# Kernel tuning notes

Hardware: AMD Instinct MI355X
Metric: run time of the kernel (lower is better)

The kernel has to match this reference:

```python
import jax, jax.numpy as jnp
import numpy as np
import math

B, S, D = 2, 8192, 1024
NW, SHIFT = 16, 256          # num_windows, shift_window
NH, DH = 16, 64              # heads = D // dim_head
DFF = 4 * D
EPS = 1e-6


def setup_inputs() -> dict:
    key = jax.random.key(0)
    ks = jax.random.split(key, 12)
    s = 1.0 / math.sqrt(D)
    return {
        "x": jax.random.normal(ks[0], (B, S, D), jnp.float32),
        "wq": jax.random.normal(ks[1], (D, NH * DH), jnp.float32) * s,
        "wk": jax.random.normal(ks[2], (D, NH * DH), jnp.float32) * s,
        "wv": jax.random.normal(ks[3], (D, NH * DH), jnp.float32) * s,
        "wo": jax.random.normal(ks[4], (NH * DH, D), jnp.float32) * s,
        "g_attn": jnp.ones((D,), jnp.float32),
        "g_ff": jnp.ones((D,), jnp.float32),
        "w1": jax.random.normal(ks[5], (D, DFF), jnp.float32) * s,
        "b1": jnp.zeros((DFF,), jnp.float32),
        "w2": jax.random.normal(ks[6], (DFF, D), jnp.float32) * (1.0 / math.sqrt(DFF)),
        "b2": jnp.zeros((D,), jnp.float32),
    }


def _rmsnorm(x, g):
    return x * g * jax.lax.rsqrt(jnp.mean(x * x, axis=-1, keepdims=True) + EPS)


def reference(x, wq, wk, wv, wo, g_attn, g_ff, w1, b1, w2, b2):
    skip = x
    h = _rmsnorm(x, g_attn)
    # shift (note: source rolls by -shift both before AND after attention)
    h = jnp.roll(h, -SHIFT, axis=1)
    # window partition: [B, NW, n, D]
    n = S // NW
    h = h.reshape(B, NW, n, D)
    q = (h @ wq).reshape(B, NW, n, NH, DH)
    k = (h @ wk).reshape(B, NW, n, NH, DH)
    v = (h @ wv).reshape(B, NW, n, NH, DH)
    scores = jnp.einsum('bwqhd,bwkhd->bwhqk', q, k) * (1.0 / math.sqrt(DH))
    a = jax.nn.softmax(scores, axis=-1)
    o = jnp.einsum('bwhqk,bwkhd->bwqhd', a, v).reshape(B, NW, n, NH * DH)
    o = (o @ wo).reshape(B, S, D)
    o = jnp.roll(o, -SHIFT, axis=1)  # faithful to source (rolls -shift again)
    x = o + skip
    skip = x
    h = _rmsnorm(x, g_ff)
    h = jax.nn.gelu(h @ w1 + b1) @ w2 + b2
    return h + skip
```

## Files before the change

### kernel.cpp

```cpp
#include <hip/hip_runtime.h>
#include <stdint.h>

#define S_LEN 8192
#define D_DIM 1024
#define SHIFT_W 256
#define NROWS 16384

typedef __bf16 bf16;
typedef __bf16 bf16x8 __attribute__((ext_vector_type(8)));
typedef __bf16 bf16x4 __attribute__((ext_vector_type(4)));
typedef float f32x4 __attribute__((ext_vector_type(4)));

typedef __attribute__((address_space(1))) const void gas_t;
typedef __attribute__((address_space(3))) void las_t;

__device__ __forceinline__ void load_lds16(const void* g, void* l) {
  __builtin_amdgcn_global_load_lds((gas_t*)g, (las_t*)l, 16, 0, 0);
}

__device__ __forceinline__ int xcd_swizzle(int orig, int nwg) {
  return (orig & 7) * (nwg >> 3) + (orig >> 3);
}

__global__ __launch_bounds__(256) void k_transpose_cvt(const float* __restrict__ in,
                                                       bf16* __restrict__ out,
                                                       int R, int C) {
  __shared__ float tile[32][33];
  int lx = threadIdx.x & 31, ly = threadIdx.x >> 5;
  int tc = blockIdx.x * 32, tr = blockIdx.y * 32;
#pragma unroll
  for (int i = 0; i < 4; i++)
    tile[ly + i * 8][lx] = in[(size_t)(tr + ly + i * 8) * C + tc + lx];
  __syncthreads();
#pragma unroll
  for (int i = 0; i < 4; i++)
    out[(size_t)(tc + ly + i * 8) * R + tr + lx] = (bf16)tile[lx][ly + i * 8];
}

__global__ __launch_bounds__(256) void k_rmsnorm(const float* __restrict__ x,
                                                 const float* __restrict__ g,
                                                 bf16* __restrict__ out, int shift) {
  int row = blockIdx.x;
  int b = row >> 13, r = row & (S_LEN - 1);
  int src = (b << 13) | ((r + shift) & (S_LEN - 1));
  int t = threadIdx.x;
  float4 v = *(const float4*)(x + (size_t)src * D_DIM + t * 4);
  float ss = v.x * v.x + v.y * v.y + v.z * v.z + v.w * v.w;
#pragma unroll
  for (int off = 32; off; off >>= 1) ss += __shfl_xor(ss, off);
  __shared__ float red[4];
  if ((t & 63) == 0) red[t >> 6] = ss;
  __syncthreads();
  ss = red[0] + red[1] + red[2] + red[3];
  float sc = rsqrtf(ss * (1.0f / D_DIM) + 1e-6f);
  float4 gv = *(const float4*)(g + t * 4);
  bf16x4 o;
  o[0] = (bf16)(v.x * gv.x * sc);
  o[1] = (bf16)(v.y * gv.y * sc);
  o[2] = (bf16)(v.z * gv.z * sc);
  o[3] = (bf16)(v.w * gv.w * sc);
  *(bf16x4*)(out + (size_t)row * D_DIM + t * 4) = o;
}

#define VM8 asm volatile("s_waitcnt vmcnt(8)" ::: "memory")
#define VM4 asm volatile("s_waitcnt vmcnt(4)" ::: "memory")
#define VM0 asm volatile("s_waitcnt vmcnt(0)" ::: "memory")
#define BAR __builtin_amdgcn_s_barrier()

#define STAGE(kbase, kk, dbuf)                                        \
  {                                                                   \
    const bf16* _ga = gAs + (kbase) + (kk) * 32;                      \
    const bf16* _gb = gBs + (kbase) + (kk) * 32;                      \
    char* _lb = smem + (dbuf) * 65536 + (kk) * 16384 + wv * 1024;     \
    load_lds16(_ga, _lb);                                             \
    load_lds16(_ga + 128 * (size_t)K, _lb + 8192);                    \
    load_lds16(_gb, _lb + 32768);                                     \
    load_lds16(_gb + 128 * (size_t)K, _lb + 40960);                   \
  }

#define DS_A(mh, kkof)                                                \
  {                                                                   \
    _Pragma("unroll") for (int mf = 0; mf < 4; mf++)                  \
        a[mf] = *(const bf16x8*)(Ac + (kkof) + aBase + (mh) * 4096 + mf * 1024); \
  }
#define DS_B(kkof)                                                    \
  {                                                                   \
    _Pragma("unroll") for (int nf = 0; nf < 4; nf++)                  \
        bfr[nf] = *(const bf16x8*)(Ac + (kkof) + bBase + nf * 1024);  \
  }
#define MFMA16(mh)                                                    \
  {                                                                   \
    __builtin_amdgcn_s_setprio(1);                                    \
    _Pragma("unroll") for (int mf = 0; mf < 4; mf++)                  \
        _Pragma("unroll") for (int nf = 0; nf < 4; nf++)              \
            acc[(mh) * 4 + mf][nf] = __builtin_amdgcn_mfma_f32_16x16x32_bf16( \
                a[mf], bfr[nf], acc[(mh) * 4 + mf][nf], 0, 0, 0);     \
    __builtin_amdgcn_s_setprio(0);                                    \
  }

template <int EPI>
__global__ __launch_bounds__(512, 2) void k_gemm(const bf16* __restrict__ A,
                                                 const bf16* __restrict__ BT,
                                                 bf16* __restrict__ obf,
                                                 float* __restrict__ of32,
                                                 const float* __restrict__ bias,
                                                 const float* __restrict__ skip,
                                                 int K, int ldc) {
  extern __shared__ char smem[];
  const int tid = threadIdx.x;
  const int wv = tid >> 6, lane = tid & 63;
  const int lr = lane & 15, lg = lane >> 4;
  const int wm = wv >> 2, wn = wv & 3;

  const int wgid = xcd_swizzle(blockIdx.x, gridDim.x);
  const int mb = wgid & 63, nb = wgid >> 6;
  const int m0 = mb * 256, n0 = nb * 256;

  const int sr = ((tid >> 6) << 4) + ((tid >> 2) & 15);
  const int skoff = (((tid & 3) ^ ((tid >> 3) & 3)) << 3);
  const bf16* gAs = A + (size_t)(m0 + sr) * K + skoff;
  const bf16* gBs = BT + (size_t)(n0 + sr) * K + skoff;

  const int kchunk = (lg ^ ((lr >> 1) & 3)) << 4;
  const int aBase = wm * 8192 + lr * 64 + kchunk;
  const int bBase = 32768 + wn * 4096 + lr * 64 + kchunk;

  f32x4 acc[8][4] = {};
  const int nt = K >> 6;

  STAGE(0, 0, 0);
  STAGE(0, 1, 0);
  STAGE(64, 0, 1);
  VM8;
  BAR;

  int cur = 0;
  for (int t = 0; t < nt; ++t) {
    const int k0 = t << 6;
    const char* Ac = smem + cur * 65536;
    bf16x8 a[4], bfr[4];
    DS_A(0, 0);
    DS_B(0);
    BAR;
    if (t + 1 < nt) STAGE(k0 + 64, 1, cur ^ 1);
    MFMA16(0);
    DS_A(1, 0);
    BAR;
    MFMA16(1);
    if (t + 1 < nt) { VM8; } else { VM0; }
    BAR;
    DS_A(0, 16384);
    DS_B(16384);
    BAR;
    if (t + 2 < nt) STAGE(k0 + 128, 0, cur);
    MFMA16(0);
    DS_A(1, 16384);
    BAR;
    MFMA16(1);
    if (t + 1 < nt) {
      if (t + 2 < nt) { VM8; } else { VM4; }
      BAR;
    }
    cur ^= 1;
  }

#pragma unroll
  for (int mh = 0; mh < 2; mh++)
#pragma unroll
    for (int mf = 0; mf < 4; mf++) {
      int row0 = m0 + wm * 128 + mh * 64 + mf * 16 + lg * 4;
#pragma unroll
      for (int nf = 0; nf < 4; nf++) {
        int col = n0 + wn * 64 + nf * 16 + lr;
#pragma unroll
        for (int ii = 0; ii < 4; ii++) {
          float c = acc[mh * 4 + mf][nf][ii];
          int r = row0 + ii;
          if constexpr (EPI == 0) {
            obf[(size_t)r * ldc + col] = (bf16)c;
          } else if constexpr (EPI == 1) {
            int b = r >> 13, rr = r & (S_LEN - 1);
            int s = (rr - SHIFT_W) & (S_LEN - 1);
            size_t o = ((size_t)((b << 13) | s)) * ldc + col;
            of32[o] = c + skip[o];
          } else if constexpr (EPI == 2) {
            float z = c + bias[col];
            float u = 0.7978845608f * (z + 0.044715f * z * z * z);
            u = fminf(fmaxf(u, -15.f), 15.f);
            float e = __expf(2.f * u);
            obf[(size_t)r * ldc + col] = (bf16)(0.5f * z * (1.f + (e - 1.f) / (e + 1.f)));
          } else {
            size_t o = (size_t)r * ldc + col;
            of32[o] = c + bias[col] + skip[o];
          }
        }
      }
    }
}

__global__ __launch_bounds__(256) void k_attn(const bf16* __restrict__ qkv,
                                              bf16* __restrict__ out) {
  __shared__ __align__(16) char Qs[8192];
  __shared__ __align__(16) char Ks[8192];
  __shared__ __align__(16) char Vs[8192];
  __shared__ __align__(16) char Ps[4][2048];
  const int tid = threadIdx.x;
  const int wave = tid >> 6, lane = tid & 63;
  const int lr = lane & 15, lg = lane >> 4;
  const int bid = xcd_swizzle(blockIdx.x, gridDim.x);
  const int qt = bid & 7;
  const int h = (bid >> 3) & 15;
  const int bw = bid >> 7;
  const int rowbase = bw * 512;
  const int qrow0 = rowbase + qt * 64;

  {
    int r = tid >> 2, c0 = tid & 3;
    const bf16* src = qkv + (size_t)(qrow0 + r) * 3072 + h * 64;
#pragma unroll
    for (int j = 0; j < 2; j++) {
      int ch = c0 + j * 4;
      uint4 val = *(const uint4*)(src + ch * 8);
      int byte = (r * 128 + ch * 16) ^ ((r & 7) << 4);
      *(uint4*)(Qs + byte) = val;
    }
  }
  __syncthreads();
  bf16x8 qf[2];
  {
    int qr = wave * 16 + lr;
#pragma unroll
    for (int kk = 0; kk < 2; kk++) {
      int byte = (qr * 128 + (kk * 32 + lg * 8) * 2) ^ ((qr & 7) << 4);
      qf[kk] = *(const bf16x8*)(Qs + byte);
    }
  }

  f32x4 oacc[4] = {};
  float m_run = -__builtin_inff(), l_run = 0.f;

  for (int kt = 0; kt < 8; ++kt) {
    __syncthreads();
    {
      int r = tid >> 2, c0 = tid & 3;
      const bf16* ksrc = qkv + (size_t)(rowbase + kt * 64 + r) * 3072 + 1024 + h * 64;
      const bf16* vsrc = ksrc + 1024;
#pragma unroll
      for (int j = 0; j < 2; j++) {
        int ch = c0 + j * 4;
        uint4 val = *(const uint4*)(ksrc + ch * 8);
        int byte = (r * 128 + ch * 16) ^ ((r & 7) << 4);
        *(uint4*)(Ks + byte) = val;
      }
#pragma unroll
      for (int j = 0; j < 2; j++) {
        int ch = c0 + j * 4;
        bf16x8 vv = *(const bf16x8*)(vsrc + ch * 8);
#pragma unroll
        for (int e = 0; e < 8; e++) {
          int d = ch * 8 + e;
          int byte = (d * 128 + r * 2) ^ ((d & 7) << 4);
          *(bf16*)(Vs + byte) = vv[e];
        }
      }
    }
    __syncthreads();
    f32x4 sc[4] = {};
#pragma unroll
    for (int kk = 0; kk < 2; kk++)
#pragma unroll
      for (int mf = 0; mf < 4; mf++) {
        int kr = mf * 16 + lr;
        int byte = (kr * 128 + (kk * 32 + lg * 8) * 2) ^ ((kr & 7) << 4);
        bf16x8 kf = *(const bf16x8*)(Ks + byte);
        sc[mf] = __builtin_amdgcn_mfma_f32_16x16x32_bf16(kf, qf[kk], sc[mf], 0, 0, 0);
      }
    float mx = -__builtin_inff();
#pragma unroll
    for (int mf = 0; mf < 4; mf++)
#pragma unroll
      for (int i = 0; i < 4; i++) mx = fmaxf(mx, sc[mf][i]);
    mx = fmaxf(mx, __shfl_xor(mx, 16));
    mx = fmaxf(mx, __shfl_xor(mx, 32));
    float mnew = fmaxf(m_run, mx);
    float alpha = __expf(0.125f * (m_run - mnew));
    float lsum = 0.f;
    float ps[4][4];
#pragma unroll
    for (int mf = 0; mf < 4; mf++)
#pragma unroll
      for (int i = 0; i < 4; i++) {
        float p = __expf(0.125f * (sc[mf][i] - mnew));
        ps[mf][i] = p;
        lsum += p;
      }
    lsum += __shfl_xor(lsum, 16);
    lsum += __shfl_xor(lsum, 32);
    l_run = l_run * alpha + lsum;
    m_run = mnew;
#pragma unroll
    for (int dm = 0; dm < 4; dm++) oacc[dm] *= alpha;
#pragma unroll
    for (int mf = 0; mf < 4; mf++) {
      bf16x4 pv;
#pragma unroll
      for (int i = 0; i < 4; i++) pv[i] = (bf16)ps[mf][i];
      int byte = (lr * 128 + (mf * 16 + lg * 4) * 2) ^ ((lr & 7) << 4);
      *(bf16x4*)(Ps[wave] + byte) = pv;
    }
#pragma unroll
    for (int kk = 0; kk < 2; kk++) {
      int pbyte = (lr * 128 + (kk * 32 + lg * 8) * 2) ^ ((lr & 7) << 4);
      bf16x8 pf = *(const bf16x8*)(Ps[wave] + pbyte);
#pragma unroll
      for (int dm = 0; dm < 4; dm++) {
        int d = dm * 16 + lr;
        int byte = (d * 128 + (kk * 32 + lg * 8) * 2) ^ ((d & 7) << 4);
        bf16x8 vf = *(const bf16x8*)(Vs + byte);
        oacc[dm] = __builtin_amdgcn_mfma_f32_16x16x32_bf16(vf, pf, oacc[dm], 0, 0, 0);
      }
    }
  }
  float inv = 1.f / l_run;
  int rowq = qrow0 + wave * 16 + lr;
#pragma unroll
  for (int dm = 0; dm < 4; dm++) {
    bf16x4 ov;
#pragma unroll
    for (int i = 0; i < 4; i++) ov[i] = (bf16)(oacc[dm][i] * inv);
    *(bf16x4*)(out + (size_t)rowq * 1024 + h * 64 + dm * 16 + lg * 4) = ov;
  }
}

extern "C" void kernel_launch(void* const* d_in, const int* in_sizes, int n_in,
                              void* d_out, int out_size, void* d_ws, size_t ws_size,
                              hipStream_t stream) {
  const float* x = (const float*)d_in[0];
  const float* wq = (const float*)d_in[1];
  const float* wk = (const float*)d_in[2];
  const float* wv = (const float*)d_in[3];
  const float* wo = (const float*)d_in[4];
  const float* ga = (const float*)d_in[5];
  const float* gf = (const float*)d_in[6];
  const float* w1 = (const float*)d_in[7];
  const float* b1 = (const float*)d_in[8];
  const float* w2 = (const float*)d_in[9];
  const float* b2 = (const float*)d_in[10];
  float* out = (float*)d_out;

  char* ws = (char*)d_ws;
  const size_t MB = 1024 * 1024;
  bf16* wqkvT = (bf16*)(ws);
  bf16* woT = (bf16*)(ws + 6 * MB);
  bf16* w1T = (bf16*)(ws + 8 * MB);
  bf16* w2T = (bf16*)(ws + 16 * MB);
  float* x1 = (float*)(ws + 24 * MB);
  bf16* hbuf = (bf16*)(ws + 88 * MB);
  bf16* qkv = (bf16*)(ws + 120 * MB);
  bf16* mid = qkv;

  (void)hipFuncSetAttribute(reinterpret_cast<const void*>(&k_gemm<0>),
                            hipFuncAttributeMaxDynamicSharedMemorySize, 131072);
  (void)hipFuncSetAttribute(reinterpret_cast<const void*>(&k_gemm<1>),
                            hipFuncAttributeMaxDynamicSharedMemorySize, 131072);
  (void)hipFuncSetAttribute(reinterpret_cast<const void*>(&k_gemm<2>),
                            hipFuncAttributeMaxDynamicSharedMemorySize, 131072);
  (void)hipFuncSetAttribute(reinterpret_cast<const void*>(&k_gemm<3>),
                            hipFuncAttributeMaxDynamicSharedMemorySize, 131072);

  k_transpose_cvt<<<dim3(32, 32), 256, 0, stream>>>(wq, wqkvT, 1024, 1024);
  k_transpose_cvt<<<dim3(32, 32), 256, 0, stream>>>(wk, wqkvT + 1024 * 1024, 1024, 1024);
  k_transpose_cvt<<<dim3(32, 32), 256, 0, stream>>>(wv, wqkvT + 2 * 1024 * 1024, 1024, 1024);
  k_transpose_cvt<<<dim3(32, 32), 256, 0, stream>>>(wo, woT, 1024, 1024);
  k_transpose_cvt<<<dim3(128, 32), 256, 0, stream>>>(w1, w1T, 1024, 4096);
  k_transpose_cvt<<<dim3(32, 128), 256, 0, stream>>>(w2, w2T, 4096, 1024);

  k_rmsnorm<<<NROWS, 256, 0, stream>>>(x, ga, hbuf, SHIFT_W);
  k_gemm<0><<<64 * 12, 512, 131072, stream>>>(hbuf, wqkvT, qkv, nullptr, nullptr, nullptr, 1024, 3072);
  k_attn<<<4096, 256, 0, stream>>>(qkv, hbuf);
  k_gemm<1><<<64 * 4, 512, 131072, stream>>>(hbuf, woT, nullptr, x1, nullptr, x, 1024, 1024);
  k_rmsnorm<<<NROWS, 256, 0, stream>>>(x1, gf, hbuf, 0);
  k_gemm<2><<<64 * 16, 512, 131072, stream>>>(hbuf, w1T, mid, nullptr, b1, nullptr, 1024, 4096);
  k_gemm<3><<<64 * 4, 512, 131072, stream>>>(mid, w2T, nullptr, out, b2, x1, 4096, 1024);
}
```

Before: 682.0 us.

## Stage GEMM epilogue through LDS for vectorized stores and remap tile order per XCD

The GEMM epilogue now writes accumulator fragments into LDS, one 64-row slab at a time, then reads them back row-contiguously. Each thread can then issue 4-wide vector loads and stores for the output, bias and skip tensors, replacing the earlier scattered scalar stores. The workgroup-to-tile mapping also changes so each XCD covers a 16x(NB/2) block of tiles, which should improve L2 reuse of A and B. The cost is extra barriers and LDS traffic in the epilogue, plus an assumption that gridDim is shaped so the new mapping covers all tiles.

```diff
diff --git a/kernel.cpp b/kernel.cpp
--- a/kernel.cpp
+++ b/kernel.cpp
@@ -112,8 +112,11 @@
   const int lr = lane & 15, lg = lane >> 4;
   const int wm = wv >> 2, wn = wv & 3;
 
-  const int wgid = xcd_swizzle(blockIdx.x, gridDim.x);
-  const int mb = wgid & 63, nb = wgid >> 6;
+  const int NB = gridDim.x >> 6;
+  const int xcd = blockIdx.x & 7;
+  const int l = blockIdx.x >> 3;
+  const int mb = ((xcd & 3) << 4) + (l & 15);
+  const int nb = (xcd >> 2) * (NB >> 1) + (l >> 4);
   const int m0 = mb * 256, n0 = nb * 256;
 
   const int sr = ((tid >> 6) << 4) + ((tid >> 2) & 15);
@@ -164,35 +167,66 @@
     cur ^= 1;
   }
 
+  float* lds_f = (float*)smem;
+  const int erow = tid >> 3;
+  const int ecol0 = (tid & 7) * 4;
 #pragma unroll
   for (int mh = 0; mh < 2; mh++)
 #pragma unroll
-    for (int mf = 0; mf < 4; mf++) {
-      int row0 = m0 + wm * 128 + mh * 64 + mf * 16 + lg * 4;
-#pragma unroll
-      for (int nf = 0; nf < 4; nf++) {
-        int col = n0 + wn * 64 + nf * 16 + lr;
-#pragma unroll
-        for (int ii = 0; ii < 4; ii++) {
-          float c = acc[mh * 4 + mf][nf][ii];
-          int r = row0 + ii;
-          if constexpr (EPI == 0) {
-            obf[(size_t)r * ldc + col] = (bf16)c;
-          } else if constexpr (EPI == 1) {
-            int b = r >> 13, rr = r & (S_LEN - 1);
-            int s = (rr - SHIFT_W) & (S_LEN - 1);
-            size_t o = ((size_t)((b << 13) | s)) * ldc + col;
-            of32[o] = c + skip[o];
-          } else if constexpr (EPI == 2) {
-            float z = c + bias[col];
+    for (int wmr = 0; wmr < 2; wmr++) {
+      BAR;
+      if (wm == wmr) {
+#pragma unroll
+        for (int mf = 0; mf < 4; mf++) {
+          int lrow = mf * 16 + lg * 4;
+#pragma unroll
+          for (int nf = 0; nf < 4; nf++) {
+            int lcol = wn * 64 + nf * 16 + lr;
+#pragma unroll
+            for (int ii = 0; ii < 4; ii++)
+              lds_f[(lrow + ii) * 260 + lcol] = acc[mh * 4 + mf][nf][ii];
+          }
+        }
+      }
+      BAR;
+      int gr = m0 + wmr * 128 + mh * 64 + erow;
+      size_t orow;
+      if constexpr (EPI == 1) {
+        int b = gr >> 13, rr = gr & (S_LEN - 1);
+        orow = (size_t)((b << 13) | ((rr - SHIFT_W) & (S_LEN - 1))) * ldc;
+      } else {
+        orow = (size_t)gr * ldc;
+      }
+#pragma unroll
+      for (int j = 0; j < 8; j++) {
+        f32x4 v = *(const f32x4*)&lds_f[erow * 260 + ecol0 + j * 32];
+        int col = n0 + ecol0 + j * 32;
+        if constexpr (EPI == 0) {
+          bf16x4 o;
+#pragma unroll
+          for (int e = 0; e < 4; e++) o[e] = (bf16)v[e];
+          *(bf16x4*)(obf + orow + col) = o;
+        } else if constexpr (EPI == 1) {
+          f32x4 s = *(const f32x4*)(skip + orow + col);
+          f32x4 r = v + s;
+          *(f32x4*)(of32 + orow + col) = r;
+        } else if constexpr (EPI == 2) {
+          f32x4 bi = *(const f32x4*)(bias + col);
+          bf16x4 o;
+#pragma unroll
+          for (int e = 0; e < 4; e++) {
+            float z = v[e] + bi[e];
             float u = 0.7978845608f * (z + 0.044715f * z * z * z);
             u = fminf(fmaxf(u, -15.f), 15.f);
-            float e = __expf(2.f * u);
-            obf[(size_t)r * ldc + col] = (bf16)(0.5f * z * (1.f + (e - 1.f) / (e + 1.f)));
-          } else {
-            size_t o = (size_t)r * ldc + col;
-            of32[o] = c + bias[col] + skip[o];
+            float ex = __expf(2.f * u);
+            o[e] = (bf16)(0.5f * z * (1.f + (ex - 1.f) / (ex + 1.f)));
           }
+          *(bf16x4*)(obf + orow + col) = o;
+        } else {
+          f32x4 bi = *(const f32x4*)(bias + col);
+          f32x4 s = *(const f32x4*)(skip + orow + col);
+          f32x4 r = v + bi + s;
+          *(f32x4*)(of32 + orow + col) = r;
         }
       }
     }
```

Result: faster. 666.1 us (-2.3%).
